# Optimization experiments

Hardware: AMD Instinct MI355X
Metric: run time of the kernel (lower is better)

Reference implementation:

```python
import jax, jax.numpy as jnp
import numpy as np
from jax import lax

TEMPERATURE = 0.5
MOMENTUM = 0.9
EPS = 1e-12  # F.normalize eps

B, D, K = 8192, 512, 16384


def _l2norm(x):
    # matches F.normalize(p=2): x / max(||x||, eps)
    n = jnp.sqrt(jnp.sum(x * x, axis=-1, keepdims=True))
    return x / jnp.maximum(n, EPS)


def setup_inputs() -> dict:
    key = jax.random.key(0)
    k1, k2, k3 = jax.random.split(key, 3)
    embeddings = jax.random.normal(k1, (B, D), dtype=jnp.float32)
    cluster_ids = jax.random.randint(k2, (B,), 0, K, dtype=jnp.int64)
    prototypes = jax.random.normal(k3, (K, D), dtype=jnp.float32)
    return {"embeddings": embeddings, "cluster_ids": cluster_ids, "prototypes": prototypes}


def reference(embeddings, cluster_ids, prototypes):
    emb_n = _l2norm(embeddings)            # [B, D]
    proto_n = _l2norm(prototypes)          # [K, D]
    sim = jnp.einsum('bd,kd->bk', emb_n, proto_n) / TEMPERATURE  # [B, K]

    pos = jnp.take_along_axis(sim, cluster_ids[:, None], axis=1)  # [B, 1]
    # mask out the positive column, then stable logsumexp over negatives
    is_pos = jnp.arange(sim.shape[1])[None, :] == cluster_ids[:, None]  # [B, K]
    neg = jnp.where(is_pos, -jnp.inf, sim)
    lse = jax.scipy.special.logsumexp(neg, axis=1, keepdims=True)       # [B, 1]
    loss = jnp.mean(-pos + lse)

    # serial momentum EMA update (order-dependent for duplicate cluster ids)
    def step(protos, xc):
        x, c = xc
        row = MOMENTUM * protos[c] + (1.0 - MOMENTUM) * x
        return protos.at[c].set(row), None

    new_protos, _ = lax.scan(step, prototypes, (embeddings, cluster_ids))
    return loss, new_protos
```

## Files before the change

kernel.cpp:

```cpp
#include <hip/hip_runtime.h>
#include <hip/hip_bf16.h>


#define B_N 8192
#define D_N 512
#define K_N 16384
#define INV_T 2.0f
#define MOM 0.9f

#define BM 128
#define BN 128
#define BKF 128
#define SPLIT 32
#define TILES ((K_N / SPLIT) / BN)
#define CHUNKS (D_N / BKF)
#define CAP 64

typedef __attribute__((ext_vector_type(8))) int intx8;
typedef __attribute__((ext_vector_type(4))) float floatx4;

__device__ __forceinline__ void gl_lds16(const void* g, void* lds) {
    __builtin_amdgcn_global_load_lds(
        (const __attribute__((address_space(1))) void*)g,
        (__attribute__((address_space(3))) void*)lds, 16, 0, 0);
}

__global__ void norm_kernel(const float* __restrict__ emb, const float* __restrict__ pro,
                            unsigned char* __restrict__ embq, unsigned char* __restrict__ proq,
                            float* __restrict__ rowsum, float* __restrict__ out) {
    if (blockIdx.x < 32) rowsum[blockIdx.x * 256 + threadIdx.x] = 0.0f;
    if (blockIdx.x == 32 && threadIdx.x == 0) out[0] = 0.0f;
    int row = blockIdx.x * 4 + (threadIdx.x >> 6);
    int lane = threadIdx.x & 63;
    const float* x;
    unsigned char* o;
    if (row < B_N) {
        x = emb + (size_t)row * D_N;
        o = embq + (size_t)row * D_N;
    } else {
        x = pro + (size_t)(row - B_N) * D_N;
        o = proq + (size_t)(row - B_N) * D_N;
    }
    const float4* xp = (const float4*)(x + lane * 8);
    float4 v0 = xp[0];
    float4 v1 = xp[1];
    float ss = v0.x * v0.x + v0.y * v0.y + v0.z * v0.z + v0.w * v0.w +
               v1.x * v1.x + v1.y * v1.y + v1.z * v1.z + v1.w * v1.w;
    #pragma unroll
    for (int of = 32; of; of >>= 1) ss += __shfl_xor(ss, of);
    float sc = 16.0f / fmaxf(sqrtf(ss), 1e-12f);
    int w0 = 0, w1 = 0;
    w0 = __builtin_amdgcn_cvt_pk_fp8_f32(v0.x * sc, v0.y * sc, w0, false);
    w0 = __builtin_amdgcn_cvt_pk_fp8_f32(v0.z * sc, v0.w * sc, w0, true);
    w1 = __builtin_amdgcn_cvt_pk_fp8_f32(v1.x * sc, v1.y * sc, w1, false);
    w1 = __builtin_amdgcn_cvt_pk_fp8_f32(v1.z * sc, v1.w * sc, w1, true);
    int2 st = {w0, w1};
    *(int2*)(o + lane * 8) = st;
}

__global__ void pos_kernel(const float* __restrict__ emb, const float* __restrict__ pro,
                           const int* __restrict__ cid, float* __restrict__ rowpos) {
    int b = blockIdx.x * 4 + (threadIdx.x >> 6);
    int lane = threadIdx.x & 63;
    int c = cid[b];
    const float4* ep = (const float4*)(emb + (size_t)b * D_N + lane * 8);
    const float4* pp = (const float4*)(pro + (size_t)c * D_N + lane * 8);
    float4 e0 = ep[0], e1 = ep[1], p0 = pp[0], p1 = pp[1];
    float dp = e0.x * p0.x + e0.y * p0.y + e0.z * p0.z + e0.w * p0.w +
               e1.x * p1.x + e1.y * p1.y + e1.z * p1.z + e1.w * p1.w;
    float ee = e0.x * e0.x + e0.y * e0.y + e0.z * e0.z + e0.w * e0.w +
               e1.x * e1.x + e1.y * e1.y + e1.z * e1.z + e1.w * e1.w;
    float qq = p0.x * p0.x + p0.y * p0.y + p0.z * p0.z + p0.w * p0.w +
               p1.x * p1.x + p1.y * p1.y + p1.z * p1.z + p1.w * p1.w;
    #pragma unroll
    for (int o = 32; o; o >>= 1) {
        dp += __shfl_xor(dp, o);
        ee += __shfl_xor(ee, o);
        qq += __shfl_xor(qq, o);
    }
    if (lane == 0)
        rowpos[b] = INV_T * dp / (fmaxf(sqrtf(ee), 1e-12f) * fmaxf(sqrtf(qq), 1e-12f));
}

__global__ __launch_bounds__(256) void flash_kernel(const unsigned char* __restrict__ embq,
                                                    const unsigned char* __restrict__ proq,
                                                    float* __restrict__ rowsum_g) {
    __shared__ __align__(16) unsigned char As[BM * BKF];
    __shared__ __align__(16) unsigned char Bs[BN * BKF];
    const int t = threadIdx.x;
    const int w = t >> 6, lane = t & 63;
    const int quad = lane >> 4, lcol = lane & 15;
    const int wm = w >> 1, wn = w & 1;
    const int rowBase = blockIdx.x * BM;
    const int nBegin = blockIdx.y * (K_N / SPLIT);

    const int fsw0 = (((quad << 1) | 0) ^ (lcol & 7)) << 4;
    const int fsw1 = (((quad << 1) | 1) ^ (lcol & 7)) << 4;
    const unsigned char* aF = &As[(wm * 64 + lcol) * BKF];
    const unsigned char* bF = &Bs[(wn * 64 + lcol) * BKF];
    const int srow = w * 8 + (lane >> 3);
    const int scol = ((lane & 7) ^ (lane >> 3)) << 4;
    const unsigned char* aS = embq + (size_t)(rowBase + srow) * D_N + scol;
    const unsigned char* bS = proq + (size_t)(nBegin + srow) * D_N + scol;

    float rowsum[16];
    #pragma unroll
    for (int i = 0; i < 16; i++) rowsum[i] = 0.0f;

    #pragma unroll
    for (int p = 0; p < 4; p++) {
        gl_lds16(aS + p * 32 * D_N, &As[p * 4096 + w * 1024]);
        gl_lds16(bS + p * 32 * D_N, &Bs[p * 4096 + w * 1024]);
    }

    for (int tile = 0; tile < TILES; tile++) {
        floatx4 acc[4][4];
        #pragma unroll
        for (int mt = 0; mt < 4; mt++)
            #pragma unroll
            for (int nt = 0; nt < 4; nt++) {
                floatx4 z = {0.0f, 0.0f, 0.0f, 0.0f};
                acc[mt][nt] = z;
            }
        #pragma unroll
        for (int ch = 0; ch < CHUNKS; ch++) {
            __syncthreads();
            intx8 af[4], bf[4];
            #pragma unroll
            for (int mt = 0; mt < 4; mt++) {
                int4 lo = *(const int4*)(aF + mt * 16 * BKF + fsw0);
                int4 hi = *(const int4*)(aF + mt * 16 * BKF + fsw1);
                intx8 v = {lo.x, lo.y, lo.z, lo.w, hi.x, hi.y, hi.z, hi.w};
                af[mt] = v;
            }
            #pragma unroll
            for (int nt = 0; nt < 4; nt++) {
                int4 lo = *(const int4*)(bF + nt * 16 * BKF + fsw0);
                int4 hi = *(const int4*)(bF + nt * 16 * BKF + fsw1);
                intx8 v = {lo.x, lo.y, lo.z, lo.w, hi.x, hi.y, hi.z, hi.w};
                bf[nt] = v;
            }
            __syncthreads();
            if (ch + 1 < CHUNKS) {
                #pragma unroll
                for (int p = 0; p < 4; p++) {
                    gl_lds16(aS + p * 32 * D_N + (ch + 1) * BKF, &As[p * 4096 + w * 1024]);
                    gl_lds16(bS + p * 32 * D_N + (ch + 1) * BKF, &Bs[p * 4096 + w * 1024]);
                }
            } else if (tile + 1 < TILES) {
                #pragma unroll
                for (int p = 0; p < 4; p++) {
                    gl_lds16(aS + p * 32 * D_N, &As[p * 4096 + w * 1024]);
                    gl_lds16(bS + (size_t)BN * D_N + p * 32 * D_N, &Bs[p * 4096 + w * 1024]);
                }
            }
            #pragma unroll
            for (int mt = 0; mt < 4; mt++)
                #pragma unroll
                for (int nt = 0; nt < 4; nt++)
                    acc[mt][nt] = __builtin_amdgcn_mfma_scale_f32_16x16x128_f8f6f4(
                        af[mt], bf[nt], acc[mt][nt], 0, 0, 0, 0x7F7F7F7F, 0, 0x7F7F7F7F);
        }
        bS += (size_t)BN * D_N;
        #pragma unroll
        for (int mt = 0; mt < 4; mt++)
            #pragma unroll
            for (int nt = 0; nt < 4; nt++)
                #pragma unroll
                for (int r = 0; r < 4; r++)
                    rowsum[mt * 4 + r] += __expf(acc[mt][nt][r] * (INV_T / 256.0f));
    }
    #pragma unroll
    for (int i = 0; i < 16; i++) {
        #pragma unroll
        for (int o = 1; o < 16; o <<= 1) rowsum[i] += __shfl_xor(rowsum[i], o);
    }
    if (lcol == 0) {
        #pragma unroll
        for (int mt = 0; mt < 4; mt++)
            #pragma unroll
            for (int r = 0; r < 4; r++)
                atomicAdd(&rowsum_g[rowBase + wm * 64 + mt * 16 + quad * 4 + r],
                          rowsum[mt * 4 + r]);
    }
}

__global__ void loss_kernel(const float* __restrict__ rowsum, const float* __restrict__ rowpos,
                            float* __restrict__ out, int* __restrict__ cnt) {
    __shared__ float red[256];
    int t = threadIdx.x;
    int b = blockIdx.x * 256 + t;
    cnt[b * 2] = 0;
    cnt[b * 2 + 1] = 0;
    float p = rowpos[b];
    red[t] = logf(rowsum[b] - __expf(p)) - p;
    __syncthreads();
    for (int o = 128; o; o >>= 1) {
        if (t < o) red[t] += red[t + o];
        __syncthreads();
    }
    if (t == 0) atomicAdd(out, red[0] * (1.0f / (float)B_N));
}

__global__ void ema_count(const int* __restrict__ cid, int* __restrict__ cnt,
                          int* __restrict__ bucket) {
    int b = blockIdx.x * 256 + threadIdx.x;
    int c = cid[b];
    int slot = atomicAdd(&cnt[c], 1);
    if (slot < CAP) bucket[c * CAP + slot] = b;
}

__global__ void ema_apply(const float* __restrict__ emb, const float* __restrict__ pro,
                          const int* __restrict__ cnt, const int* __restrict__ bucket,
                          float* __restrict__ outp) {
    int k = blockIdx.x * 4 + (threadIdx.x >> 6);
    int lane = threadIdx.x & 63;
    int n = cnt[k];
    n = n < CAP ? n : CAP;
    const float4* pp = (const float4*)(pro + (size_t)k * D_N + lane * 8);
    float4 a0 = pp[0], a1 = pp[1];
    int myb = (lane < n) ? bucket[k * CAP + lane] : 0x7fffffff;
    for (int i = 0; i < n; i++) {
        int m = myb;
        #pragma unroll
        for (int o = 1; o < 64; o <<= 1) {
            int v = __shfl_xor(m, o);
            m = v < m ? v : m;
        }
        const float4* ep = (const float4*)(emb + (size_t)m * D_N + lane * 8);
        float4 e0 = ep[0], e1 = ep[1];
        a0.x = MOM * a0.x + (1.0f - MOM) * e0.x;
        a0.y = MOM * a0.y + (1.0f - MOM) * e0.y;
        a0.z = MOM * a0.z + (1.0f - MOM) * e0.z;
        a0.w = MOM * a0.w + (1.0f - MOM) * e0.w;
        a1.x = MOM * a1.x + (1.0f - MOM) * e1.x;
        a1.y = MOM * a1.y + (1.0f - MOM) * e1.y;
        a1.z = MOM * a1.z + (1.0f - MOM) * e1.z;
        a1.w = MOM * a1.w + (1.0f - MOM) * e1.w;
        if (myb == m) myb = 0x7fffffff;
    }
    float4* op = (float4*)(outp + (size_t)k * D_N + lane * 8);
    op[0] = a0;
    op[1] = a1;
}

extern "C" void kernel_launch(void* const* d_in, const int* in_sizes, int n_in,
                              void* d_out, int out_size, void* d_ws, size_t ws_size,
                              hipStream_t stream) {
    const float* emb = (const float*)d_in[0];
    const int* cid = (const int*)d_in[1];
    const float* pro = (const float*)d_in[2];
    float* out = (float*)d_out;

    char* ws = (char*)d_ws;
    unsigned char* embq = (unsigned char*)ws;
    unsigned char* proq = (unsigned char*)(ws + 4194304);
    float* rowsum = (float*)(ws + 12582912);
    float* rowpos = (float*)(ws + 12615680);
    int* cnt = (int*)(ws + 4194304);
    int* bucket = (int*)(ws + 4194304 + 65536);

    norm_kernel<<<(B_N + K_N) / 4, 256, 0, stream>>>(emb, pro, embq, proq, rowsum, out);
    pos_kernel<<<B_N / 4, 256, 0, stream>>>(emb, pro, cid, rowpos);
    flash_kernel<<<dim3(B_N / BM, SPLIT), 256, 0, stream>>>(embq, proq, rowsum);
    loss_kernel<<<B_N / 256, 256, 0, stream>>>(rowsum, rowpos, out, cnt);
    ema_count<<<B_N / 256, 256, 0, stream>>>(cid, cnt, bucket);
    ema_apply<<<K_N / 4, 256, 0, stream>>>(emb, pro, cnt, bucket, out + 1);
}
```

Baseline: 204.4 us.

## Rewrite FP8 flash GEMM with 256x256 tiles, double-buffered LDS and phased MFMA

```diff
diff --git a/kernel.cpp b/kernel.cpp
--- a/kernel.cpp
+++ b/kernel.cpp
@@ -8,12 +8,11 @@
 #define INV_T 2.0f
 #define MOM 0.9f
 
-#define BM 128
-#define BN 128
+#define BM 256
+#define BN 256
 #define BKF 128
-#define SPLIT 32
-#define TILES ((K_N / SPLIT) / BN)
-#define CHUNKS (D_N / BKF)
+#define CT 4
+#define NT (CT * 4)
 #define CAP 64
 
 typedef __attribute__((ext_vector_type(8))) int intx8;
@@ -82,106 +81,183 @@
         rowpos[b] = INV_T * dp / (fmaxf(sqrtf(ee), 1e-12f) * fmaxf(sqrtf(qq), 1e-12f));
 }
 
-__global__ __launch_bounds__(256) void flash_kernel(const unsigned char* __restrict__ embq,
-                                                    const unsigned char* __restrict__ proq,
-                                                    float* __restrict__ rowsum_g) {
-    __shared__ __align__(16) unsigned char As[BM * BKF];
-    __shared__ __align__(16) unsigned char Bs[BN * BKF];
+__global__ __launch_bounds__(512, 2) void flash_kernel(const unsigned char* __restrict__ embq,
+                                                       const unsigned char* __restrict__ proq,
+                                                       float* __restrict__ rowsum_g) {
+    __shared__ __align__(16) unsigned char As[2][BM * BKF];
+    __shared__ __align__(16) unsigned char Bs[2][BN * BKF];
     const int t = threadIdx.x;
     const int w = t >> 6, lane = t & 63;
     const int quad = lane >> 4, lcol = lane & 15;
-    const int wm = w >> 1, wn = w & 1;
+    const int wm = w >> 2, wn = w & 3;
     const int rowBase = blockIdx.x * BM;
-    const int nBegin = blockIdx.y * (K_N / SPLIT);
+    const int nBase = blockIdx.y * (BN * CT);
 
     const int fsw0 = (((quad << 1) | 0) ^ (lcol & 7)) << 4;
     const int fsw1 = (((quad << 1) | 1) ^ (lcol & 7)) << 4;
-    const unsigned char* aF = &As[(wm * 64 + lcol) * BKF];
-    const unsigned char* bF = &Bs[(wn * 64 + lcol) * BKF];
+    const int aOff = (wm * 128 + lcol) * BKF;
+    const int bOff = (wn * 64 + lcol) * BKF;
+
     const int srow = w * 8 + (lane >> 3);
     const int scol = ((lane & 7) ^ (lane >> 3)) << 4;
     const unsigned char* aS = embq + (size_t)(rowBase + srow) * D_N + scol;
-    const unsigned char* bS = proq + (size_t)(nBegin + srow) * D_N + scol;
-
-    float rowsum[16];
-    #pragma unroll
-    for (int i = 0; i < 16; i++) rowsum[i] = 0.0f;
-
-    #pragma unroll
-    for (int p = 0; p < 4; p++) {
-        gl_lds16(aS + p * 32 * D_N, &As[p * 4096 + w * 1024]);
-        gl_lds16(bS + p * 32 * D_N, &Bs[p * 4096 + w * 1024]);
-    }
-
-    for (int tile = 0; tile < TILES; tile++) {
-        floatx4 acc[4][4];
-        #pragma unroll
-        for (int mt = 0; mt < 4; mt++)
-            #pragma unroll
-            for (int nt = 0; nt < 4; nt++) {
-                floatx4 z = {0.0f, 0.0f, 0.0f, 0.0f};
-                acc[mt][nt] = z;
+    const unsigned char* bS = proq + (size_t)(nBase + srow) * D_N + scol;
+    const int ldsW = w * 1024;
+
+    auto issueA = [&](int st, unsigned char* buf) {
+        const unsigned char* s0 = aS + (st & 3) * BKF;
+        #pragma unroll
+        for (int p = 0; p < 4; p++)
+            gl_lds16(s0 + (size_t)p * 64 * D_N, buf + ldsW + p * 8192);
+    };
+    auto issueB2 = [&](int st, unsigned char* buf, int h) {
+        const unsigned char* s0 =
+            bS + (size_t)(st >> 2) * (BN * D_N) + (st & 3) * BKF + (size_t)(h * 2) * 64 * D_N;
+        #pragma unroll
+        for (int p = 0; p < 2; p++)
+            gl_lds16(s0 + (size_t)p * 64 * D_N, buf + ldsW + (h * 2 + p) * 8192);
+    };
+    auto readA = [&](const unsigned char* base, int mq, intx8* af) {
+        #pragma unroll
+        for (int i = 0; i < 4; i++) {
+            const unsigned char* rp = base + aOff + (mq * 64 + i * 16) * BKF;
+            int4 lo = *(const int4*)(rp + fsw0);
+            int4 hi = *(const int4*)(rp + fsw1);
+            intx8 v = {lo.x, lo.y, lo.z, lo.w, hi.x, hi.y, hi.z, hi.w};
+            af[i] = v;
+        }
+    };
+    auto readB = [&](const unsigned char* base, int nq, intx8* bf) {
+        #pragma unroll
+        for (int j = 0; j < 2; j++) {
+            const unsigned char* rp = base + bOff + (nq * 32 + j * 16) * BKF;
+            int4 lo = *(const int4*)(rp + fsw0);
+            int4 hi = *(const int4*)(rp + fsw1);
+            intx8 v = {lo.x, lo.y, lo.z, lo.w, hi.x, hi.y, hi.z, hi.w};
+            bf[j] = v;
+        }
+    };
+
+    floatx4 acc[8][4];
+    float rs[32];
+    #pragma unroll
+    for (int mt = 0; mt < 8; mt++)
+        #pragma unroll
+        for (int nt = 0; nt < 4; nt++) {
+            floatx4 z = {0.0f, 0.0f, 0.0f, 0.0f};
+            acc[mt][nt] = z;
+        }
+    #pragma unroll
+    for (int i = 0; i < 32; i++) rs[i] = 0.0f;
+
+    issueA(0, As[0]);
+    issueB2(0, Bs[0], 0);
+    issueB2(0, Bs[0], 1);
+    issueA(1, As[1]);
+    asm volatile("s_waitcnt vmcnt(4)" ::: "memory");
+    __builtin_amdgcn_s_barrier();
+
+    #pragma unroll
+    for (int s = 0; s < NT; s++) {
+        unsigned char* cA = As[s & 1];
+        unsigned char* cB = Bs[s & 1];
+        unsigned char* nB = Bs[(s + 1) & 1];
+        intx8 af[4], bf[2];
+
+        readA(cA, 0, af);
+        readB(cB, 0, bf);
+        if (s + 1 < NT) issueB2(s + 1, nB, 0);
+        __builtin_amdgcn_s_barrier();
+        asm volatile("s_waitcnt lgkmcnt(0)" ::: "memory");
+        __builtin_amdgcn_sched_barrier(0);
+        __builtin_amdgcn_s_setprio(1);
+        #pragma unroll
+        for (int i = 0; i < 4; i++)
+            #pragma unroll
+            for (int j = 0; j < 2; j++)
+                acc[i][j] = __builtin_amdgcn_mfma_scale_f32_16x16x128_f8f6f4(
+                    af[i], bf[j], acc[i][j], 0, 0, 0, 0x7F7F7F7F, 0, 0x7F7F7F7F);
+        __builtin_amdgcn_s_setprio(0);
+        __builtin_amdgcn_s_barrier();
+
+        readB(cB, 1, bf);
+        if (s + 1 < NT) issueB2(s + 1, nB, 1);
+        __builtin_amdgcn_s_barrier();
+        asm volatile("s_waitcnt lgkmcnt(0)" ::: "memory");
+        __builtin_amdgcn_sched_barrier(0);
+        __builtin_amdgcn_s_setprio(1);
+        #pragma unroll
+        for (int i = 0; i < 4; i++)
+            #pragma unroll
+            for (int j = 0; j < 2; j++)
+                acc[i][2 + j] = __builtin_amdgcn_mfma_scale_f32_16x16x128_f8f6f4(
+                    af[i], bf[j], acc[i][2 + j], 0, 0, 0, 0x7F7F7F7F, 0, 0x7F7F7F7F);
+        __builtin_amdgcn_s_setprio(0);
+        __builtin_amdgcn_s_barrier();
+
+        readA(cA, 1, af);
+        readB(cB, 0, bf);
+        __builtin_amdgcn_s_barrier();
+        asm volatile("s_waitcnt lgkmcnt(0)" ::: "memory");
+        __builtin_amdgcn_sched_barrier(0);
+        __builtin_amdgcn_s_setprio(1);
+        #pragma unroll
+        for (int i = 0; i < 4; i++)
+            #pragma unroll
+            for (int j = 0; j < 2; j++)
+                acc[4 + i][j] = __builtin_amdgcn_mfma_scale_f32_16x16x128_f8f6f4(
+                    af[i], bf[j], acc[4 + i][j], 0, 0, 0, 0x7F7F7F7F, 0, 0x7F7F7F7F);
+        __builtin_amdgcn_s_setprio(0);
+        __builtin_amdgcn_s_barrier();
+
+        readB(cB, 1, bf);
+        __builtin_amdgcn_s_barrier();
+        asm volatile("s_waitcnt lgkmcnt(0)" ::: "memory");
+        __builtin_amdgcn_sched_barrier(0);
+        __builtin_amdgcn_s_setprio(1);
+        #pragma unroll
+        for (int i = 0; i < 4; i++)
+            #pragma unroll
+            for (int j = 0; j < 2; j++)
+                acc[4 + i][2 + j] = __builtin_amdgcn_mfma_scale_f32_16x16x128_f8f6f4(
+                    af[i], bf[j], acc[4 + i][2 + j], 0, 0, 0, 0x7F7F7F7F, 0, 0x7F7F7F7F);
+        __builtin_amdgcn_s_setprio(0);
+
+        if (s + 1 < NT) {
+            if (s + 2 < NT) {
+                issueA(s + 2, cA);
+                asm volatile("s_waitcnt vmcnt(4)" ::: "memory");
+            } else {
+                asm volatile("s_waitcnt vmcnt(0)" ::: "memory");
             }
-        #pragma unroll
-        for (int ch = 0; ch < CHUNKS; ch++) {
-            __syncthreads();
-            intx8 af[4], bf[4];
-            #pragma unroll
-            for (int mt = 0; mt < 4; mt++) {
-                int4 lo = *(const int4*)(aF + mt * 16 * BKF + fsw0);
-                int4 hi = *(const int4*)(aF + mt * 16 * BKF + fsw1);
-                intx8 v = {lo.x, lo.y, lo.z, lo.w, hi.x, hi.y, hi.z, hi.w};
-                af[mt] = v;
-            }
-            #pragma unroll
-            for (int nt = 0; nt < 4; nt++) {
-                int4 lo = *(const int4*)(bF + nt * 16 * BKF + fsw0);
-                int4 hi = *(const int4*)(bF + nt * 16 * BKF + fsw1);
-                intx8 v = {lo.x, lo.y, lo.z, lo.w, hi.x, hi.y, hi.z, hi.w};
-                bf[nt] = v;
-            }
-            __syncthreads();
-            if (ch + 1 < CHUNKS) {
-                #pragma unroll
-                for (int p = 0; p < 4; p++) {
-                    gl_lds16(aS + p * 32 * D_N + (ch + 1) * BKF, &As[p * 4096 + w * 1024]);
-                    gl_lds16(bS + p * 32 * D_N + (ch + 1) * BKF, &Bs[p * 4096 + w * 1024]);
-                }
-            } else if (tile + 1 < TILES) {
-                #pragma unroll
-                for (int p = 0; p < 4; p++) {
-                    gl_lds16(aS + p * 32 * D_N, &As[p * 4096 + w * 1024]);
-                    gl_lds16(bS + (size_t)BN * D_N + p * 32 * D_N, &Bs[p * 4096 + w * 1024]);
-                }
-            }
-            #pragma unroll
-            for (int mt = 0; mt < 4; mt++)
+            __builtin_amdgcn_s_barrier();
+        }
+
+        if ((s & 3) == 3) {
+            #pragma unroll
+            for (int mt = 0; mt < 8; mt++)
                 #pragma unroll
                 for (int nt = 0; nt < 4; nt++)
-                    acc[mt][nt] = __builtin_amdgcn_mfma_scale_f32_16x16x128_f8f6f4(
-                        af[mt], bf[nt], acc[mt][nt], 0, 0, 0, 0x7F7F7F7F, 0, 0x7F7F7F7F);
-        }
-        bS += (size_t)BN * D_N;
-        #pragma unroll
-        for (int mt = 0; mt < 4; mt++)
-            #pragma unroll
-            for (int nt = 0; nt < 4; nt++)
-                #pragma unroll
-                for (int r = 0; r < 4; r++)
-                    rowsum[mt * 4 + r] += __expf(acc[mt][nt][r] * (INV_T / 256.0f));
-    }
-    #pragma unroll
-    for (int i = 0; i < 16; i++) {
-        #pragma unroll
-        for (int o = 1; o < 16; o <<= 1) rowsum[i] += __shfl_xor(rowsum[i], o);
+                    #pragma unroll
+                    for (int r = 0; r < 4; r++) {
+                        rs[mt * 4 + r] += __expf(acc[mt][nt][r] * (INV_T / 256.0f));
+                        acc[mt][nt][r] = 0.0f;
+                    }
+        }
+    }
+
+    #pragma unroll
+    for (int i = 0; i < 32; i++) {
+        #pragma unroll
+        for (int o = 1; o < 16; o <<= 1) rs[i] += __shfl_xor(rs[i], o);
     }
     if (lcol == 0) {
         #pragma unroll
-        for (int mt = 0; mt < 4; mt++)
+        for (int mt = 0; mt < 8; mt++)
             #pragma unroll
             for (int r = 0; r < 4; r++)
-                atomicAdd(&rowsum_g[rowBase + wm * 64 + mt * 16 + quad * 4 + r],
-                          rowsum[mt * 4 + r]);
+                atomicAdd(&rowsum_g[rowBase + wm * 128 + mt * 16 + quad * 4 + r],
+                          rs[mt * 4 + r]);
     }
 }
 
@@ -262,7 +338,7 @@
 
     norm_kernel<<<(B_N + K_N) / 4, 256, 0, stream>>>(emb, pro, embq, proq, rowsum, out);
     pos_kernel<<<B_N / 4, 256, 0, stream>>>(emb, pro, cid, rowpos);
-    flash_kernel<<<dim3(B_N / BM, SPLIT), 256, 0, stream>>>(embq, proq, rowsum);
+    flash_kernel<<<dim3(B_N / BM, K_N / (BN * CT)), 512, 0, stream>>>(embq, proq, rowsum);
     loss_kernel<<<B_N / 256, 256, 0, stream>>>(rowsum, rowpos, out, cnt);
     ema_count<<<B_N / 256, 256, 0, stream>>>(cid, cnt, bucket);
     ema_apply<<<K_N / 4, 256, 0, stream>>>(emb, pro, cnt, bucket, out + 1);
```

Result: slower. 251.6 us (+23.1%).

## Keep full A tile resident in LDS and double-buffer B chunks with 512 threads

Applied to the files above, without the earlier changes.

```diff
diff --git a/kernel.cpp b/kernel.cpp
--- a/kernel.cpp
+++ b/kernel.cpp
@@ -9,11 +9,10 @@
 #define MOM 0.9f
 
 #define BM 128
-#define BN 128
 #define BKF 128
-#define SPLIT 32
-#define TILES ((K_N / SPLIT) / BN)
-#define CHUNKS (D_N / BKF)
+#define BTR 256
+#define KSPLIT 4
+#define NCH 64
 #define CAP 64
 
 typedef __attribute__((ext_vector_type(8))) int intx8;
@@ -23,6 +22,13 @@
     __builtin_amdgcn_global_load_lds(
         (const __attribute__((address_space(1))) void*)g,
         (__attribute__((address_space(3))) void*)lds, 16, 0, 0);
+}
+
+__device__ __forceinline__ intx8 frag2(const unsigned char* rp, int o0, int o1) {
+    intx8 v;
+    ((int4*)&v)[0] = *(const int4*)(rp + o0);
+    ((int4*)&v)[1] = *(const int4*)(rp + o1);
+    return v;
 }
 
 __global__ void norm_kernel(const float* __restrict__ emb, const float* __restrict__ pro,
@@ -82,106 +88,114 @@
         rowpos[b] = INV_T * dp / (fmaxf(sqrtf(ee), 1e-12f) * fmaxf(sqrtf(qq), 1e-12f));
 }
 
-__global__ __launch_bounds__(256) void flash_kernel(const unsigned char* __restrict__ embq,
-                                                    const unsigned char* __restrict__ proq,
-                                                    float* __restrict__ rowsum_g) {
-    __shared__ __align__(16) unsigned char As[BM * BKF];
-    __shared__ __align__(16) unsigned char Bs[BN * BKF];
+__global__ __launch_bounds__(512, 2) void flash_kernel(const unsigned char* __restrict__ embq,
+                                                       const unsigned char* __restrict__ proq,
+                                                       float* __restrict__ rowsum_g) {
+    __shared__ __align__(16) unsigned char As[BM * D_N];
+    __shared__ __align__(16) unsigned char Bs[2][BTR * BKF];
     const int t = threadIdx.x;
     const int w = t >> 6, lane = t & 63;
     const int quad = lane >> 4, lcol = lane & 15;
-    const int wm = w >> 1, wn = w & 1;
+    const int wm = w >> 2, wn = w & 3;
     const int rowBase = blockIdx.x * BM;
-    const int nBegin = blockIdx.y * (K_N / SPLIT);
+    const int kb = blockIdx.y * (K_N / KSPLIT);
 
     const int fsw0 = (((quad << 1) | 0) ^ (lcol & 7)) << 4;
     const int fsw1 = (((quad << 1) | 1) ^ (lcol & 7)) << 4;
-    const unsigned char* aF = &As[(wm * 64 + lcol) * BKF];
-    const unsigned char* bF = &Bs[(wn * 64 + lcol) * BKF];
-    const int srow = w * 8 + (lane >> 3);
-    const int scol = ((lane & 7) ^ (lane >> 3)) << 4;
-    const unsigned char* aS = embq + (size_t)(rowBase + srow) * D_N + scol;
-    const unsigned char* bS = proq + (size_t)(nBegin + srow) * D_N + scol;
-
-    float rowsum[16];
-    #pragma unroll
-    for (int i = 0; i < 16; i++) rowsum[i] = 0.0f;
-
-    #pragma unroll
-    for (int p = 0; p < 4; p++) {
-        gl_lds16(aS + p * 32 * D_N, &As[p * 4096 + w * 1024]);
-        gl_lds16(bS + p * 32 * D_N, &Bs[p * 4096 + w * 1024]);
-    }
-
-    for (int tile = 0; tile < TILES; tile++) {
-        floatx4 acc[4][4];
-        #pragma unroll
-        for (int mt = 0; mt < 4; mt++)
-            #pragma unroll
-            for (int nt = 0; nt < 4; nt++) {
-                floatx4 z = {0.0f, 0.0f, 0.0f, 0.0f};
-                acc[mt][nt] = z;
-            }
-        #pragma unroll
-        for (int ch = 0; ch < CHUNKS; ch++) {
-            __syncthreads();
-            intx8 af[4], bf[4];
-            #pragma unroll
-            for (int mt = 0; mt < 4; mt++) {
-                int4 lo = *(const int4*)(aF + mt * 16 * BKF + fsw0);
-                int4 hi = *(const int4*)(aF + mt * 16 * BKF + fsw1);
-                intx8 v = {lo.x, lo.y, lo.z, lo.w, hi.x, hi.y, hi.z, hi.w};
-                af[mt] = v;
-            }
-            #pragma unroll
-            for (int nt = 0; nt < 4; nt++) {
-                int4 lo = *(const int4*)(bF + nt * 16 * BKF + fsw0);
-                int4 hi = *(const int4*)(bF + nt * 16 * BKF + fsw1);
-                intx8 v = {lo.x, lo.y, lo.z, lo.w, hi.x, hi.y, hi.z, hi.w};
-                bf[nt] = v;
-            }
-            __syncthreads();
-            if (ch + 1 < CHUNKS) {
+    const unsigned char* aF = As + (size_t)(wm * 64 + lcol) * D_N;
+    const int ldsW = w * 1024;
+
+    const int aRow = w * 2 + (lane >> 5);
+    const unsigned char* aS = embq + (size_t)(rowBase + aRow) * D_N +
+                              (((lane >> 3) & 3) << 7) + (((lane & 7) ^ (aRow & 7)) << 4);
+    const unsigned char* bS = proq + (size_t)(kb + w * 8 + (lane >> 3)) * D_N +
+                              (((lane & 7) ^ ((lane >> 3) & 7)) << 4);
+
+    floatx4 acc[4][4];
+    float rs[16];
+    #pragma unroll
+    for (int i = 0; i < 4; i++)
+        #pragma unroll
+        for (int j = 0; j < 4; j++) {
+            floatx4 z = {0.0f, 0.0f, 0.0f, 0.0f};
+            acc[i][j] = z;
+        }
+    #pragma unroll
+    for (int i = 0; i < 16; i++) rs[i] = 0.0f;
+
+    #pragma unroll
+    for (int p = 0; p < 8; p++)
+        gl_lds16(aS + p * 8192, As + p * 8192 + ldsW);
+    #pragma unroll
+    for (int p = 0; p < 4; p++)
+        gl_lds16(bS + (size_t)p * 64 * D_N, Bs[0] + p * 8192 + ldsW);
+    #pragma unroll
+    for (int p = 0; p < 4; p++)
+        gl_lds16(bS + (size_t)p * 64 * D_N + BKF, Bs[1] + p * 8192 + ldsW);
+    asm volatile("s_waitcnt vmcnt(4)" ::: "memory");
+    __builtin_amdgcn_s_barrier();
+
+    for (int cc = 0; cc < NCH; cc++) {
+        const unsigned char* bufc = Bs[cc & 1];
+        const unsigned char* ra = aF + ((cc & 3) << 7);
+        const unsigned char* rb = bufc + (size_t)(wn * 64 + lcol) * BKF;
+
+        intx8 af[4], bf[4];
+        #pragma unroll
+        for (int i = 0; i < 4; i++)
+            af[i] = frag2(ra + i * (16 * D_N), fsw0, fsw1);
+        #pragma unroll
+        for (int j = 0; j < 4; j++)
+            bf[j] = frag2(rb + j * (16 * BKF), fsw0, fsw1);
+
+        __builtin_amdgcn_s_setprio(1);
+        #pragma unroll
+        for (int i = 0; i < 4; i++)
+            #pragma unroll
+            for (int j = 0; j < 4; j++)
+                acc[i][j] = __builtin_amdgcn_mfma_scale_f32_16x16x128_f8f6f4(
+                    af[i], bf[j], acc[i][j], 0, 0, 0, 0x7F7F7F7F, 0, 0x7F7F7F7F);
+        __builtin_amdgcn_s_setprio(0);
+
+        if ((cc & 3) == 3) {
+            #pragma unroll
+            for (int i = 0; i < 4; i++)
                 #pragma unroll
-                for (int p = 0; p < 4; p++) {
-                    gl_lds16(aS + p * 32 * D_N + (ch + 1) * BKF, &As[p * 4096 + w * 1024]);
-                    gl_lds16(bS + p * 32 * D_N + (ch + 1) * BKF, &Bs[p * 4096 + w * 1024]);
-                }
-            } else if (tile + 1 < TILES) {
-                #pragma unroll
-                for (int p = 0; p < 4; p++) {
-                    gl_lds16(aS + p * 32 * D_N, &As[p * 4096 + w * 1024]);
-                    gl_lds16(bS + (size_t)BN * D_N + p * 32 * D_N, &Bs[p * 4096 + w * 1024]);
-                }
-            }
-            #pragma unroll
-            for (int mt = 0; mt < 4; mt++)
-                #pragma unroll
-                for (int nt = 0; nt < 4; nt++)
-                    acc[mt][nt] = __builtin_amdgcn_mfma_scale_f32_16x16x128_f8f6f4(
-                        af[mt], bf[nt], acc[mt][nt], 0, 0, 0, 0x7F7F7F7F, 0, 0x7F7F7F7F);
-        }
-        bS += (size_t)BN * D_N;
-        #pragma unroll
-        for (int mt = 0; mt < 4; mt++)
-            #pragma unroll
-            for (int nt = 0; nt < 4; nt++)
-                #pragma unroll
-                for (int r = 0; r < 4; r++)
-                    rowsum[mt * 4 + r] += __expf(acc[mt][nt][r] * (INV_T / 256.0f));
-    }
+                for (int j = 0; j < 4; j++)
+                    #pragma unroll
+                    for (int r = 0; r < 4; r++) {
+                        rs[i * 4 + r] += __expf(acc[i][j][r] * (INV_T / 256.0f));
+                        acc[i][j][r] = 0.0f;
+                    }
+        }
+
+        asm volatile("s_barrier" ::: "memory");
+        if (cc + 2 < NCH) {
+            const unsigned char* s =
+                bS + (size_t)(((cc + 2) >> 2) * BTR) * D_N + (((cc + 2) & 3) << 7);
+            unsigned char* d = (unsigned char*)Bs[cc & 1] + ldsW;
+            #pragma unroll
+            for (int p = 0; p < 4; p++)
+                gl_lds16(s + (size_t)p * 64 * D_N, d + p * 8192);
+            asm volatile("s_waitcnt vmcnt(4)" ::: "memory");
+        } else {
+            asm volatile("s_waitcnt vmcnt(0)" ::: "memory");
+        }
+        asm volatile("s_barrier" ::: "memory");
+    }
+
     #pragma unroll
     for (int i = 0; i < 16; i++) {
         #pragma unroll
-        for (int o = 1; o < 16; o <<= 1) rowsum[i] += __shfl_xor(rowsum[i], o);
+        for (int o = 1; o < 16; o <<= 1) rs[i] += __shfl_xor(rs[i], o);
     }
     if (lcol == 0) {
         #pragma unroll
-        for (int mt = 0; mt < 4; mt++)
+        for (int i = 0; i < 4; i++)
             #pragma unroll
             for (int r = 0; r < 4; r++)
-                atomicAdd(&rowsum_g[rowBase + wm * 64 + mt * 16 + quad * 4 + r],
-                          rowsum[mt * 4 + r]);
+                atomicAdd(&rowsum_g[rowBase + wm * 64 + i * 16 + quad * 4 + r],
+                          rs[i * 4 + r]);
     }
 }
 
@@ -262,7 +276,7 @@
 
     norm_kernel<<<(B_N + K_N) / 4, 256, 0, stream>>>(emb, pro, embq, proq, rowsum, out);
     pos_kernel<<<B_N / 4, 256, 0, stream>>>(emb, pro, cid, rowpos);
-    flash_kernel<<<dim3(B_N / BM, SPLIT), 256, 0, stream>>>(embq, proq, rowsum);
+    flash_kernel<<<dim3(B_N / BM, KSPLIT), 512, 0, stream>>>(embq, proq, rowsum);
     loss_kernel<<<B_N / 256, 256, 0, stream>>>(rowsum, rowpos, out, cnt);
     ema_count<<<B_N / 256, 256, 0, stream>>>(cid, cnt, bucket);
     ema_apply<<<K_N / 4, 256, 0, stream>>>(emb, pro, cnt, bucket, out + 1);
```

Result: slower. 222.7 us (+9.0%).
